# Kernel tuning notes

Hardware: AMD Instinct MI355X
Metric: run time of the kernel (lower is better)

## Reference

```python
import jax, jax.numpy as jnp
import numpy as np

B, S, D_IN, D_OUT = 4, 2048, 4096, 4096


def setup_inputs() -> dict:
    key = jax.random.key(0)
    k1, k2, k3, k4 = jax.random.split(key, 4)
    x = jax.random.normal(k1, (B, S, D_IN), dtype=jnp.float32)
    # int8-valued weights stored as int32 (values in [-127, 127])
    weight_int8 = jax.random.randint(k2, (D_OUT, D_IN), -127, 128, dtype=jnp.int32)
    # per-output-channel scale, strictly positive (abs-max / 127 style)
    scale = jax.random.uniform(k3, (D_OUT, 1), dtype=jnp.float32, minval=1e-4, maxval=2e-2)
    bias = jax.random.normal(k4, (D_OUT,), dtype=jnp.float32)
    return {"x": x, "weight_int8": weight_int8, "scale": scale, "bias": bias}


def reference(x, weight_int8, scale, bias):
    # Dequantize: per-output-row scale applied to int8 weights -> fp32 [O, I]
    w = weight_int8.astype(jnp.float32) * scale
    # F.linear: y = x @ w^T + b
    out = jnp.einsum('bsi,oi->bso', x, w) + bias
    return out
```

## Files before the change

### kernel.cpp

```cpp
#include <hip/hip_runtime.h>
#include <cstdint>
#include <cstddef>

typedef int i32x4 __attribute__((ext_vector_type(4)));

#define BM 256
#define BN 256
#define BK 64

__device__ __forceinline__ void load16_to_lds(const void* g, void* l) {
  __builtin_amdgcn_global_load_lds(
      (const __attribute__((address_space(1))) void*)g,
      (__attribute__((address_space(3))) void*)l,
      16, 0, 0);
}

__global__ __launch_bounds__(256) void quant_xw(const float* __restrict__ x,
                                                char* __restrict__ xq,
                                                float* __restrict__ sx,
                                                const int* __restrict__ w,
                                                char* __restrict__ wq,
                                                int M, int K) {
  const int wid = blockIdx.x * 4 + (threadIdx.x >> 6);
  const int l   = threadIdx.x & 63;
  if (wid < M) {
    const float4* xr = (const float4*)(x + (size_t)wid * K);
    float4 v[16];
    float amax = 0.f;
#pragma unroll
    for (int j = 0; j < 16; ++j) {
      v[j] = xr[j * 64 + l];
      amax = fmaxf(amax, fmaxf(fmaxf(fabsf(v[j].x), fabsf(v[j].y)),
                               fmaxf(fabsf(v[j].z), fabsf(v[j].w))));
    }
#pragma unroll
    for (int off = 32; off; off >>= 1)
      amax = fmaxf(amax, __shfl_xor(amax, off));
    amax = fmaxf(amax, 1e-20f);

    const float s = 127.0f / amax;
    int* outw = (int*)(xq + (size_t)wid * K);
#pragma unroll
    for (int j = 0; j < 16; ++j) {
      int q0 = __float2int_rn(v[j].x * s);
      int q1 = __float2int_rn(v[j].y * s);
      int q2 = __float2int_rn(v[j].z * s);
      int q3 = __float2int_rn(v[j].w * s);
      outw[j * 64 + l] = (q0 & 0xff) | ((q1 & 0xff) << 8) |
                         ((q2 & 0xff) << 16) | ((q3 & 0xff) << 24);
    }
    if (l == 0) sx[wid] = amax * (1.0f / 127.0f);
  } else {
    const int r = wid - M;
    const int4* wr = (const int4*)(w + (size_t)r * K);
    int* outw = (int*)(wq + (size_t)r * K);
#pragma unroll
    for (int j = 0; j < 16; ++j) {
      int4 a = wr[j * 64 + l];
      outw[j * 64 + l] = (a.x & 0xff) | ((a.y & 0xff) << 8) |
                         ((a.z & 0xff) << 16) | ((a.w & 0xff) << 24);
    }
  }
}

__global__ __launch_bounds__(1024) void gemm_i8_bt(const char* __restrict__ A,
                                                   const char* __restrict__ Bw,
                                                   const float* __restrict__ sx,
                                                   const float* __restrict__ sw,
                                                   const float* __restrict__ bias,
                                                   float* __restrict__ out,
                                                   int M, int N, int K) {
  __shared__ __align__(16) char As[2][BM * BK];
  __shared__ __align__(16) char Bs[2][BN * BK];

  const int tid  = threadIdx.x;
  const int wave = tid >> 6;
  const int lane = tid & 63;
  const int wm   = wave >> 2;
  const int wn   = wave & 3;

  const int gx   = N / BN;
  const int nwg  = gx * (M / BM);
  const int orig = blockIdx.y * gx + blockIdx.x;
  const int wg   = (orig & 7) * (nwg >> 3) + (orig >> 3);
  const int bn   = wg % gx;
  const int bm   = wg / gx;

  i32x4 acc[4][4] = {};

  const int rowT = tid >> 2;
  const int jg   = ((tid & 3) ^ ((tid >> 3) & 3)) << 4;
  const char* Ag = A  + (size_t)(bm * BM + rowT) * K + jg;
  const char* Bg = Bw + (size_t)(bn * BN + rowT) * K + jg;

  const int ldsO = wave << 10;

  const int fr  = lane & 15;
  const int swz = (((lane >> 4) ^ ((fr >> 1) & 3)) << 4);
  int offA[4], offB[4];
#pragma unroll
  for (int m = 0; m < 4; ++m) offA[m] = (wm * 64 + m * 16 + fr) * 64 + swz;
#pragma unroll
  for (int n = 0; n < 4; ++n) offB[n] = (wn * 64 + n * 16 + fr) * 64 + swz;

  const int NT = K / BK;

  load16_to_lds(Ag, &As[0][ldsO]);
  load16_to_lds(Bg, &Bs[0][ldsO]);
  asm volatile("s_waitcnt vmcnt(0)" ::: "memory");
  __builtin_amdgcn_s_barrier();

  int buf = 0;
  for (int t = 0; t < NT; ++t) {
    const int  nb = buf ^ 1;
    const size_t ko = (size_t)(t + 1) * BK;
    const bool pf = (t + 1) < NT;

    i32x4 a0 = *(const i32x4*)&As[buf][offA[0]];
    i32x4 a1 = *(const i32x4*)&As[buf][offA[1]];
    i32x4 b0 = *(const i32x4*)&Bs[buf][offB[0]];
    i32x4 b1 = *(const i32x4*)&Bs[buf][offB[1]];
    i32x4 b2 = *(const i32x4*)&Bs[buf][offB[2]];
    i32x4 b3 = *(const i32x4*)&Bs[buf][offB[3]];
    if (pf) load16_to_lds(Ag + ko, &As[nb][ldsO]);
    __builtin_amdgcn_s_barrier();
    asm volatile("s_waitcnt lgkmcnt(0)" ::: "memory");
    __builtin_amdgcn_sched_barrier(0);
    __builtin_amdgcn_s_setprio(1);
    acc[0][0] = __builtin_amdgcn_mfma_i32_16x16x64_i8(a0, b0, acc[0][0], 0, 0, 0);
    acc[0][1] = __builtin_amdgcn_mfma_i32_16x16x64_i8(a0, b1, acc[0][1], 0, 0, 0);
    acc[0][2] = __builtin_amdgcn_mfma_i32_16x16x64_i8(a0, b2, acc[0][2], 0, 0, 0);
    acc[0][3] = __builtin_amdgcn_mfma_i32_16x16x64_i8(a0, b3, acc[0][3], 0, 0, 0);
    acc[1][0] = __builtin_amdgcn_mfma_i32_16x16x64_i8(a1, b0, acc[1][0], 0, 0, 0);
    acc[1][1] = __builtin_amdgcn_mfma_i32_16x16x64_i8(a1, b1, acc[1][1], 0, 0, 0);
    acc[1][2] = __builtin_amdgcn_mfma_i32_16x16x64_i8(a1, b2, acc[1][2], 0, 0, 0);
    acc[1][3] = __builtin_amdgcn_mfma_i32_16x16x64_i8(a1, b3, acc[1][3], 0, 0, 0);
    __builtin_amdgcn_s_setprio(0);
    __builtin_amdgcn_s_barrier();

    i32x4 a2 = *(const i32x4*)&As[buf][offA[2]];
    i32x4 a3 = *(const i32x4*)&As[buf][offA[3]];
    if (pf) load16_to_lds(Bg + ko, &Bs[nb][ldsO]);
    __builtin_amdgcn_s_barrier();
    asm volatile("s_waitcnt lgkmcnt(0)" ::: "memory");
    __builtin_amdgcn_sched_barrier(0);
    __builtin_amdgcn_s_setprio(1);
    acc[2][0] = __builtin_amdgcn_mfma_i32_16x16x64_i8(a2, b0, acc[2][0], 0, 0, 0);
    acc[2][1] = __builtin_amdgcn_mfma_i32_16x16x64_i8(a2, b1, acc[2][1], 0, 0, 0);
    acc[2][2] = __builtin_amdgcn_mfma_i32_16x16x64_i8(a2, b2, acc[2][2], 0, 0, 0);
    acc[2][3] = __builtin_amdgcn_mfma_i32_16x16x64_i8(a2, b3, acc[2][3], 0, 0, 0);
    acc[3][0] = __builtin_amdgcn_mfma_i32_16x16x64_i8(a3, b0, acc[3][0], 0, 0, 0);
    acc[3][1] = __builtin_amdgcn_mfma_i32_16x16x64_i8(a3, b1, acc[3][1], 0, 0, 0);
    acc[3][2] = __builtin_amdgcn_mfma_i32_16x16x64_i8(a3, b2, acc[3][2], 0, 0, 0);
    acc[3][3] = __builtin_amdgcn_mfma_i32_16x16x64_i8(a3, b3, acc[3][3], 0, 0, 0);
    __builtin_amdgcn_s_setprio(0);

    if (pf) { asm volatile("s_waitcnt vmcnt(0)" ::: "memory"); }
    __builtin_amdgcn_s_barrier();

    buf = nb;
  }

  const int colc = lane & 15;
  const int rq   = (lane >> 4) << 2;
  float sxv[4][4];
#pragma unroll
  for (int m = 0; m < 4; ++m) {
    const int row0 = bm * BM + wm * 64 + m * 16 + rq;
#pragma unroll
    for (int r = 0; r < 4; ++r) sxv[m][r] = sx[row0 + r];
  }
#pragma unroll
  for (int n = 0; n < 4; ++n) {
    const int col = bn * BN + wn * 64 + n * 16 + colc;
    const float sc = sw[col];
    const float bi = bias[col];
#pragma unroll
    for (int m = 0; m < 4; ++m) {
      const int row0 = bm * BM + wm * 64 + m * 16 + rq;
#pragma unroll
      for (int r = 0; r < 4; ++r)
        out[(size_t)(row0 + r) * N + col] = (float)acc[m][n][r] * (sxv[m][r] * sc) + bi;
    }
  }
}

extern "C" void kernel_launch(void* const* d_in, const int* in_sizes, int n_in,
                              void* d_out, int out_size, void* d_ws, size_t ws_size,
                              hipStream_t stream) {
  const float* x     = (const float*)d_in[0];
  const int*   w     = (const int*)d_in[1];
  const float* scale = (const float*)d_in[2];
  const float* bias  = (const float*)d_in[3];
  float*       out   = (float*)d_out;

  const int N = in_sizes[3];
  const int K = in_sizes[1] / N;
  const int M = in_sizes[0] / K;

  char*  xq = (char*)d_ws;
  char*  wq = xq + (size_t)M * K;
  float* sx = (float*)(wq + (size_t)N * K);

  const unsigned nwaves = (unsigned)(M + N);
  quant_xw<<<dim3(nwaves / 4), dim3(256), 0, stream>>>(x, xq, sx, w, wq, M, K);

  gemm_i8_bt<<<dim3(N / BN, M / BM), dim3(1024), 0, stream>>>(xq, wq, sx, scale, bias, out, M, N, K);
}
```

Measured before the change: 415.6 us.

## Use 8 waves with 128x64 warp tiles and triple-buffered LDS pipeline

Halves the workgroup to 512 threads so each wave computes a 128x64 output tile (32 accumulators), doubling register reuse of B fragments. LDS goes from double to triple buffering, so global-to-LDS loads are issued two tiles ahead. Fragment reads for the next tile are software-pipelined into the current tile's second MFMA half. This raises register pressure and LDS use (96KB), which may limit occupancy.

```diff
diff --git a/kernel.cpp b/kernel.cpp
--- a/kernel.cpp
+++ b/kernel.cpp
@@ -63,15 +63,15 @@
   }
 }
 
-__global__ __launch_bounds__(1024) void gemm_i8_bt(const char* __restrict__ A,
-                                                   const char* __restrict__ Bw,
-                                                   const float* __restrict__ sx,
-                                                   const float* __restrict__ sw,
-                                                   const float* __restrict__ bias,
-                                                   float* __restrict__ out,
-                                                   int M, int N, int K) {
-  __shared__ __align__(16) char As[2][BM * BK];
-  __shared__ __align__(16) char Bs[2][BN * BK];
+__global__ __launch_bounds__(512) void gemm_i8_bt(const char* __restrict__ A,
+                                                  const char* __restrict__ Bw,
+                                                  const float* __restrict__ sx,
+                                                  const float* __restrict__ sw,
+                                                  const float* __restrict__ bias,
+                                                  float* __restrict__ out,
+                                                  int M, int N, int K) {
+  __shared__ __align__(16) char As[3][BM * BK];
+  __shared__ __align__(16) char Bs[3][BN * BK];
 
   const int tid  = threadIdx.x;
   const int wave = tid >> 6;
@@ -86,87 +86,139 @@
   const int bn   = wg % gx;
   const int bm   = wg / gx;
 
-  i32x4 acc[4][4] = {};
+  i32x4 acc[8][4] = {};
 
   const int rowT = tid >> 2;
   const int jg   = ((tid & 3) ^ ((tid >> 3) & 3)) << 4;
-  const char* Ag = A  + (size_t)(bm * BM + rowT) * K + jg;
-  const char* Bg = Bw + (size_t)(bn * BN + rowT) * K + jg;
-
-  const int ldsO = wave << 10;
+  const char* Ag1 = A  + (size_t)(bm * BM + rowT) * K + jg;
+  const char* Ag2 = Ag1 + (size_t)128 * K;
+  const char* Bg1 = Bw + (size_t)(bn * BN + rowT) * K + jg;
+  const char* Bg2 = Bg1 + (size_t)128 * K;
+
+  const int ldsO1 = wave << 10;
+  const int ldsO2 = 8192 + (wave << 10);
 
   const int fr  = lane & 15;
   const int swz = (((lane >> 4) ^ ((fr >> 1) & 3)) << 4);
-  int offA[4], offB[4];
-#pragma unroll
-  for (int m = 0; m < 4; ++m) offA[m] = (wm * 64 + m * 16 + fr) * 64 + swz;
+  int offA[8], offB[4];
+#pragma unroll
+  for (int m = 0; m < 8; ++m) offA[m] = (wm * 128 + m * 16 + fr) * 64 + swz;
 #pragma unroll
   for (int n = 0; n < 4; ++n) offB[n] = (wn * 64 + n * 16 + fr) * 64 + swz;
 
   const int NT = K / BK;
 
-  load16_to_lds(Ag, &As[0][ldsO]);
-  load16_to_lds(Bg, &Bs[0][ldsO]);
-  asm volatile("s_waitcnt vmcnt(0)" ::: "memory");
+  load16_to_lds(Ag1,      &As[0][ldsO1]);
+  load16_to_lds(Ag2,      &As[0][ldsO2]);
+  load16_to_lds(Bg1,      &Bs[0][ldsO1]);
+  load16_to_lds(Bg2,      &Bs[0][ldsO2]);
+  load16_to_lds(Ag1 + BK, &As[1][ldsO1]);
+  load16_to_lds(Ag2 + BK, &As[1][ldsO2]);
+  load16_to_lds(Bg1 + BK, &Bs[1][ldsO1]);
+  load16_to_lds(Bg2 + BK, &Bs[1][ldsO2]);
+  asm volatile("s_waitcnt vmcnt(4)" ::: "memory");
   __builtin_amdgcn_s_barrier();
 
-  int buf = 0;
-  for (int t = 0; t < NT; ++t) {
-    const int  nb = buf ^ 1;
-    const size_t ko = (size_t)(t + 1) * BK;
-    const bool pf = (t + 1) < NT;
-
-    i32x4 a0 = *(const i32x4*)&As[buf][offA[0]];
-    i32x4 a1 = *(const i32x4*)&As[buf][offA[1]];
-    i32x4 b0 = *(const i32x4*)&Bs[buf][offB[0]];
-    i32x4 b1 = *(const i32x4*)&Bs[buf][offB[1]];
-    i32x4 b2 = *(const i32x4*)&Bs[buf][offB[2]];
-    i32x4 b3 = *(const i32x4*)&Bs[buf][offB[3]];
-    if (pf) load16_to_lds(Ag + ko, &As[nb][ldsO]);
-    __builtin_amdgcn_s_barrier();
-    asm volatile("s_waitcnt lgkmcnt(0)" ::: "memory");
-    __builtin_amdgcn_sched_barrier(0);
-    __builtin_amdgcn_s_setprio(1);
-    acc[0][0] = __builtin_amdgcn_mfma_i32_16x16x64_i8(a0, b0, acc[0][0], 0, 0, 0);
-    acc[0][1] = __builtin_amdgcn_mfma_i32_16x16x64_i8(a0, b1, acc[0][1], 0, 0, 0);
-    acc[0][2] = __builtin_amdgcn_mfma_i32_16x16x64_i8(a0, b2, acc[0][2], 0, 0, 0);
-    acc[0][3] = __builtin_amdgcn_mfma_i32_16x16x64_i8(a0, b3, acc[0][3], 0, 0, 0);
-    acc[1][0] = __builtin_amdgcn_mfma_i32_16x16x64_i8(a1, b0, acc[1][0], 0, 0, 0);
-    acc[1][1] = __builtin_amdgcn_mfma_i32_16x16x64_i8(a1, b1, acc[1][1], 0, 0, 0);
-    acc[1][2] = __builtin_amdgcn_mfma_i32_16x16x64_i8(a1, b2, acc[1][2], 0, 0, 0);
-    acc[1][3] = __builtin_amdgcn_mfma_i32_16x16x64_i8(a1, b3, acc[1][3], 0, 0, 0);
-    __builtin_amdgcn_s_setprio(0);
-    __builtin_amdgcn_s_barrier();
-
-    i32x4 a2 = *(const i32x4*)&As[buf][offA[2]];
-    i32x4 a3 = *(const i32x4*)&As[buf][offA[3]];
-    if (pf) load16_to_lds(Bg + ko, &Bs[nb][ldsO]);
-    __builtin_amdgcn_s_barrier();
-    asm volatile("s_waitcnt lgkmcnt(0)" ::: "memory");
-    __builtin_amdgcn_sched_barrier(0);
-    __builtin_amdgcn_s_setprio(1);
-    acc[2][0] = __builtin_amdgcn_mfma_i32_16x16x64_i8(a2, b0, acc[2][0], 0, 0, 0);
-    acc[2][1] = __builtin_amdgcn_mfma_i32_16x16x64_i8(a2, b1, acc[2][1], 0, 0, 0);
-    acc[2][2] = __builtin_amdgcn_mfma_i32_16x16x64_i8(a2, b2, acc[2][2], 0, 0, 0);
-    acc[2][3] = __builtin_amdgcn_mfma_i32_16x16x64_i8(a2, b3, acc[2][3], 0, 0, 0);
-    acc[3][0] = __builtin_amdgcn_mfma_i32_16x16x64_i8(a3, b0, acc[3][0], 0, 0, 0);
-    acc[3][1] = __builtin_amdgcn_mfma_i32_16x16x64_i8(a3, b1, acc[3][1], 0, 0, 0);
-    acc[3][2] = __builtin_amdgcn_mfma_i32_16x16x64_i8(a3, b2, acc[3][2], 0, 0, 0);
-    acc[3][3] = __builtin_amdgcn_mfma_i32_16x16x64_i8(a3, b3, acc[3][3], 0, 0, 0);
-    __builtin_amdgcn_s_setprio(0);
-
-    if (pf) { asm volatile("s_waitcnt vmcnt(0)" ::: "memory"); }
-    __builtin_amdgcn_s_barrier();
-
-    buf = nb;
-  }
+  i32x4 xa[4], xb[4], ya[4], yb[4];
+#pragma unroll
+  for (int m = 0; m < 4; ++m) xa[m] = *(const i32x4*)&As[0][offA[m]];
+#pragma unroll
+  for (int n = 0; n < 4; ++n) xb[n] = *(const i32x4*)&Bs[0][offB[n]];
+
+#define TILE_STEP(T, CA, CB, NA, NB)                                               \
+  {                                                                                \
+    const int    buf = (T) % 3;                                                    \
+    const int    nbf = ((T) + 2) % 3;                                              \
+    const int    nxf = ((T) + 1) % 3;                                              \
+    const size_t ko  = (size_t)((T) + 2) * BK;                                     \
+    const bool   pf  = (T) + 2 < NT;                                               \
+    const bool   rd  = (T) + 1 < NT;                                               \
+                                                                 \
+    if (pf) {                                                                      \
+      load16_to_lds(Ag1 + ko, &As[nbf][ldsO1]);                                    \
+      load16_to_lds(Ag2 + ko, &As[nbf][ldsO2]);                                    \
+    }                                                                              \
+    __builtin_amdgcn_s_barrier();                                                  \
+    asm volatile("s_waitcnt lgkmcnt(0)" ::: "memory");                             \
+    __builtin_amdgcn_sched_barrier(0);                                             \
+    __builtin_amdgcn_s_setprio(1);                                                 \
+    i32x4 a4 = *(const i32x4*)&As[buf][offA[4]];                                   \
+    i32x4 a5 = *(const i32x4*)&As[buf][offA[5]];                                   \
+    i32x4 a6 = *(const i32x4*)&As[buf][offA[6]];                                   \
+    i32x4 a7 = *(const i32x4*)&As[buf][offA[7]];                                   \
+    acc[0][0] = __builtin_amdgcn_mfma_i32_16x16x64_i8(CA[0], CB[0], acc[0][0], 0, 0, 0); \
+    acc[0][1] = __builtin_amdgcn_mfma_i32_16x16x64_i8(CA[0], CB[1], acc[0][1], 0, 0, 0); \
+    acc[0][2] = __builtin_amdgcn_mfma_i32_16x16x64_i8(CA[0], CB[2], acc[0][2], 0, 0, 0); \
+    acc[0][3] = __builtin_amdgcn_mfma_i32_16x16x64_i8(CA[0], CB[3], acc[0][3], 0, 0, 0); \
+    acc[1][0] = __builtin_amdgcn_mfma_i32_16x16x64_i8(CA[1], CB[0], acc[1][0], 0, 0, 0); \
+    acc[1][1] = __builtin_amdgcn_mfma_i32_16x16x64_i8(CA[1], CB[1], acc[1][1], 0, 0, 0); \
+    acc[1][2] = __builtin_amdgcn_mfma_i32_16x16x64_i8(CA[1], CB[2], acc[1][2], 0, 0, 0); \
+    acc[1][3] = __builtin_amdgcn_mfma_i32_16x16x64_i8(CA[1], CB[3], acc[1][3], 0, 0, 0); \
+    acc[2][0] = __builtin_amdgcn_mfma_i32_16x16x64_i8(CA[2], CB[0], acc[2][0], 0, 0, 0); \
+    acc[2][1] = __builtin_amdgcn_mfma_i32_16x16x64_i8(CA[2], CB[1], acc[2][1], 0, 0, 0); \
+    acc[2][2] = __builtin_amdgcn_mfma_i32_16x16x64_i8(CA[2], CB[2], acc[2][2], 0, 0, 0); \
+    acc[2][3] = __builtin_amdgcn_mfma_i32_16x16x64_i8(CA[2], CB[3], acc[2][3], 0, 0, 0); \
+    acc[3][0] = __builtin_amdgcn_mfma_i32_16x16x64_i8(CA[3], CB[0], acc[3][0], 0, 0, 0); \
+    acc[3][1] = __builtin_amdgcn_mfma_i32_16x16x64_i8(CA[3], CB[1], acc[3][1], 0, 0, 0); \
+    acc[3][2] = __builtin_amdgcn_mfma_i32_16x16x64_i8(CA[3], CB[2], acc[3][2], 0, 0, 0); \
+    acc[3][3] = __builtin_amdgcn_mfma_i32_16x16x64_i8(CA[3], CB[3], acc[3][3], 0, 0, 0); \
+    __builtin_amdgcn_s_setprio(0);                                                 \
+    __builtin_amdgcn_sched_barrier(0);                                             \
+    __builtin_amdgcn_s_barrier();                                                  \
+                                                                 \
+    if (pf) {                                                                      \
+      load16_to_lds(Bg1 + ko, &Bs[nbf][ldsO1]);                                    \
+      load16_to_lds(Bg2 + ko, &Bs[nbf][ldsO2]);                                    \
+    }                                                                              \
+    if (pf)      { asm volatile("s_waitcnt vmcnt(4)" ::: "memory"); }              \
+    else if (rd) { asm volatile("s_waitcnt vmcnt(0)" ::: "memory"); }              \
+    __builtin_amdgcn_s_barrier();                                                  \
+    asm volatile("s_waitcnt lgkmcnt(0)" ::: "memory");                             \
+    __builtin_amdgcn_sched_barrier(0);                                             \
+    __builtin_amdgcn_s_setprio(1);                                                 \
+    if (rd) {                                                                      \
+      NA[0] = *(const i32x4*)&As[nxf][offA[0]];                                    \
+      NA[1] = *(const i32x4*)&As[nxf][offA[1]];                                    \
+      NA[2] = *(const i32x4*)&As[nxf][offA[2]];                                    \
+      NA[3] = *(const i32x4*)&As[nxf][offA[3]];                                    \
+      NB[0] = *(const i32x4*)&Bs[nxf][offB[0]];                                    \
+      NB[1] = *(const i32x4*)&Bs[nxf][offB[1]];                                    \
+      NB[2] = *(const i32x4*)&Bs[nxf][offB[2]];                                    \
+      NB[3] = *(const i32x4*)&Bs[nxf][offB[3]];                                    \
+    }                                                                              \
+    acc[4][0] = __builtin_amdgcn_mfma_i32_16x16x64_i8(a4, CB[0], acc[4][0], 0, 0, 0); \
+    acc[4][1] = __builtin_amdgcn_mfma_i32_16x16x64_i8(a4, CB[1], acc[4][1], 0, 0, 0); \
+    acc[4][2] = __builtin_amdgcn_mfma_i32_16x16x64_i8(a4, CB[2], acc[4][2], 0, 0, 0); \
+    acc[4][3] = __builtin_amdgcn_mfma_i32_16x16x64_i8(a4, CB[3], acc[4][3], 0, 0, 0); \
+    acc[5][0] = __builtin_amdgcn_mfma_i32_16x16x64_i8(a5, CB[0], acc[5][0], 0, 0, 0); \
+    acc[5][1] = __builtin_amdgcn_mfma_i32_16x16x64_i8(a5, CB[1], acc[5][1], 0, 0, 0); \
+    acc[5][2] = __builtin_amdgcn_mfma_i32_16x16x64_i8(a5, CB[2], acc[5][2], 0, 0, 0); \
+    acc[5][3] = __builtin_amdgcn_mfma_i32_16x16x64_i8(a5, CB[3], acc[5][3], 0, 0, 0); \
+    acc[6][0] = __builtin_amdgcn_mfma_i32_16x16x64_i8(a6, CB[0], acc[6][0], 0, 0, 0); \
+    acc[6][1] = __builtin_amdgcn_mfma_i32_16x16x64_i8(a6, CB[1], acc[6][1], 0, 0, 0); \
+    acc[6][2] = __builtin_amdgcn_mfma_i32_16x16x64_i8(a6, CB[2], acc[6][2], 0, 0, 0); \
+    acc[6][3] = __builtin_amdgcn_mfma_i32_16x16x64_i8(a6, CB[3], acc[6][3], 0, 0, 0); \
+    acc[7][0] = __builtin_amdgcn_mfma_i32_16x16x64_i8(a7, CB[0], acc[7][0], 0, 0, 0); \
+    acc[7][1] = __builtin_amdgcn_mfma_i32_16x16x64_i8(a7, CB[1], acc[7][1], 0, 0, 0); \
+    acc[7][2] = __builtin_amdgcn_mfma_i32_16x16x64_i8(a7, CB[2], acc[7][2], 0, 0, 0); \
+    acc[7][3] = __builtin_amdgcn_mfma_i32_16x16x64_i8(a7, CB[3], acc[7][3], 0, 0, 0); \
+    __builtin_amdgcn_s_setprio(0);                                                 \
+    __builtin_amdgcn_sched_barrier(0);                                             \
+    __builtin_amdgcn_s_barrier();                                                  \
+  }
+
+  for (int t = 0; t < NT; t += 2) {
+    TILE_STEP(t,     xa, xb, ya, yb);
+    TILE_STEP(t + 1, ya, yb, xa, xb);
+  }
+#undef TILE_STEP
 
   const int colc = lane & 15;
   const int rq   = (lane >> 4) << 2;
-  float sxv[4][4];
-#pragma unroll
-  for (int m = 0; m < 4; ++m) {
-    const int row0 = bm * BM + wm * 64 + m * 16 + rq;
+  float sxv[8][4];
+#pragma unroll
+  for (int m = 0; m < 8; ++m) {
+    const int row0 = bm * BM + wm * 128 + m * 16 + rq;
 #pragma unroll
     for (int r = 0; r < 4; ++r) sxv[m][r] = sx[row0 + r];
   }
@@ -176,8 +228,8 @@
     const float sc = sw[col];
     const float bi = bias[col];
 #pragma unroll
-    for (int m = 0; m < 4; ++m) {
-      const int row0 = bm * BM + wm * 64 + m * 16 + rq;
+    for (int m = 0; m < 8; ++m) {
+      const int row0 = bm * BM + wm * 128 + m * 16 + rq;
 #pragma unroll
       for (int r = 0; r < 4; ++r)
         out[(size_t)(row0 + r) * N + col] = (float)acc[m][n][r] * (sxv[m][r] * sc) + bi;
@@ -205,5 +257,5 @@
   const unsigned nwaves = (unsigned)(M + N);
   quant_xw<<<dim3(nwaves / 4), dim3(256), 0, stream>>>(x, xq, sx, w, wq, M, K);
 
-  gemm_i8_bt<<<dim3(N / BN, M / BM), dim3(1024), 0, stream>>>(xq, wq, sx, scale, bias, out, M, N, K);
-}
+  gemm_i8_bt<<<dim3(N / BN, M / BM), dim3(512), 0, stream>>>(xq, wq, sx, scale, bias, out, M, N, K);
+}
```

New measurement: 463.6 us. +11.5%, slower.
